# Optimization experiments

Hardware: AMD Instinct MI355X
Metric: run time of the kernel (lower is better)

The kernel has to match this reference:

```python
import jax, jax.numpy as jnp
import numpy as np

B, C, W, H, NH, FF, L = 4, 200, 300, 128, 8, 512, 2
PH = H // NH
MAXLEN = 200
PE_N = 512
NEG = -1e15


def _sinusoidal_pe():
    # fairseq-style sinusoidal table, get_embedding(512, hidden_size)
    half = H // 2
    freq = np.exp(np.arange(half, dtype=np.float64) * -(np.log(10000.0) / (half - 1)))
    ang = np.arange(PE_N, dtype=np.float64)[:, None] * freq[None, :]
    return jnp.asarray(np.concatenate([np.sin(ang), np.cos(ang)], axis=1), jnp.float32)

PE = _sinusoidal_pe()  # [512, H], frozen (requires_grad=False in torch)


def setup_inputs() -> dict:
    key = jax.random.key(0)
    ks = jax.random.split(key, 20)

    def lin(k, fan_in, shape):
        lim = 1.0 / np.sqrt(fan_in)
        return jax.random.uniform(k, shape, jnp.float32, -lim, lim)

    return {
        'chars': jax.random.normal(ks[0], (B, C, H), jnp.float32),
        'words': jax.random.normal(ks[1], (B, W, H), jnp.float32),
        'pos_s': jax.random.randint(ks[2], (B, C), 0, MAXLEN),
        'pos_e': jax.random.randint(ks[3], (B, C), 0, MAXLEN),
        'lex_s': jax.random.randint(ks[4], (B, W), 0, MAXLEN),
        'lex_e': jax.random.randint(ks[5], (B, W), 0, MAXLEN),
        'seq_len': jax.random.randint(ks[6], (B,), 100, C + 1),
        'lex_num': jax.random.randint(ks[7], (B,), 150, W + 1),
        # Four_Pos_Fusion 'ff': Linear(4H -> H) + ReLU
        'Wf': lin(ks[8], 4 * H, (4 * H, H)),
        'bf': jnp.zeros((H,), jnp.float32),
        # per-layer attention / FFN params, stacked on leading layer dim
        'Wq': lin(ks[9], H, (L, H, H)),  'bq': jnp.zeros((L, H), jnp.float32),
        'Wk': lin(ks[10], H, (L, H, H)), 'bk': jnp.zeros((L, H), jnp.float32),
        'Wv': lin(ks[11], H, (L, H, H)), 'bv': jnp.zeros((L, H), jnp.float32),
        'Wr': lin(ks[12], H, (L, H, H)), 'br': jnp.zeros((L, H), jnp.float32),
        'u_bias': jax.random.normal(ks[13], (L, NH, PH), jnp.float32) * 0.02,
        'v_bias': jax.random.normal(ks[14], (L, NH, PH), jnp.float32) * 0.02,
        'ln1_g': jnp.ones((L, H), jnp.float32), 'ln1_b': jnp.zeros((L, H), jnp.float32),
        'ln2_g': jnp.ones((L, H), jnp.float32), 'ln2_b': jnp.zeros((L, H), jnp.float32),
        'W1': lin(ks[15], H, (L, H, FF)),  'b1': jnp.zeros((L, FF), jnp.float32),
        'W2': lin(ks[16], FF, (L, FF, H)), 'b2': jnp.zeros((L, H), jnp.float32),
    }


def _ln(x, g, b):
    m = jnp.mean(x, -1, keepdims=True)
    v = jnp.var(x, -1, keepdims=True)
    return (x - m) / jnp.sqrt(v + 1e-5) * g + b


def reference(chars, words, pos_s, pos_e, lex_s, lex_e, seq_len, lex_num,
              Wf, bf, Wq, bq, Wk, bk, Wv, bv, Wr, br, u_bias, v_bias,
              ln1_g, ln1_b, ln2_g, ln2_b, W1, b1, W2, b2):
    # four relative-position distance tables (char span vs word span), offset by max_seq_len
    idx = lambda p, l: jnp.clip(p[:, :, None] - l[:, None, :] + MAXLEN, 0, PE_N - 1)
    # Linear(4H->H) over the concat of four gathered PE tensors, expressed as
    # a sum of 4 chunked matmuls to avoid materializing the [B,C,W,4H] concat.
    rel = (PE[idx(pos_s, lex_s)] @ Wf[0:H] + PE[idx(pos_s, lex_e)] @ Wf[H:2 * H]
           + PE[idx(pos_e, lex_s)] @ Wf[2 * H:3 * H] + PE[idx(pos_e, lex_e)] @ Wf[3 * H:4 * H] + bf)
    rel = jax.nn.relu(rel)  # [B, C, W, H]

    # char_lex_len_to_mask: valid (char i, word j) pairs
    mask = (jnp.arange(C) < seq_len[:, None])[:, :, None] & (jnp.arange(W) < lex_num[:, None])[:, None, :]
    mask = mask[:, None]  # [B, 1, C, W]

    out = chars
    for i in range(L):
        q = (out @ Wq[i] + bq[i]).reshape(B, C, NH, PH)
        k = (words @ Wk[i] + bk[i]).reshape(B, W, NH, PH)
        v = (words @ Wv[i] + bv[i]).reshape(B, W, NH, PH)
        r = (rel @ Wr[i] + br[i]).reshape(B, C, W, NH, PH)
        A_C = jnp.einsum('bcnp,bwnp->bncw', q + u_bias[i], k)
        B_D = jnp.einsum('bcnp,bcwnp->bncw', q + v_bias[i], r)
        score = jnp.where(mask, A_C + B_D, NEG)  # scale=False
        att = jax.nn.softmax(score, axis=-1)
        att = jnp.where(mask, att, 0.0)  # dropout=0 (eval)
        ctx = jnp.einsum('bncw,bwnp->bcnp', att, v).reshape(B, C, H)
        out = _ln(ctx + out, ln1_g[i], ln1_b[i])
        ff = jax.nn.relu(out @ W1[i] + b1[i]) @ W2[i] + b2[i]
        out = _ln(ff + out, ln2_g[i], ln2_b[i])
    return out
```

## Files before the change

kernel.cpp:

```cpp
#include <hip/hip_runtime.h>
#include <math.h>

#define B_ 4
#define C_ 200
#define CH_ 100
#define W_ 300
#define WP_ 304
#define H_ 128
#define NH_ 8
#define PH_ 16
#define FF_ 512
#define L_ 2
#define MAXLEN_ 200
#define PEN_ 512
#define WVS_ 136
#define NTILE_ 19

typedef __bf16 bf16x8 __attribute__((ext_vector_type(8)));
typedef float f32x4v __attribute__((ext_vector_type(4)));

#define SEG_PEW   64
#define SEG_KV    (SEG_PEW + 200)
#define SEG_WR    (SEG_KV + 256)
#define SEG_W1T   (SEG_WR + 128)
#define PREP_BLOCKS (SEG_W1T + 128)

__global__ __launch_bounds__(128) void prep_kernel(
        const float* __restrict__ Wf, const float* __restrict__ bfv,
        const float* __restrict__ words,
        const float* __restrict__ Wk, const float* __restrict__ bk,
        const float* __restrict__ Wv, const float* __restrict__ bv,
        const float* __restrict__ Wr, const float* __restrict__ W1,
        const float* __restrict__ W2,
        __bf16* __restrict__ kb, __bf16* __restrict__ PEWb, __bf16* __restrict__ vTb,
        __bf16* __restrict__ WrB, __bf16* __restrict__ W1T, __bf16* __restrict__ W2T) {
    __shared__ __align__(16) float s_buf[12 * H_];
    __shared__ __align__(16) __bf16 s_vt[128][12];
    __shared__ float s_tile[32][33];
    int t = threadIdx.x;
    if (blockIdx.x < SEG_PEW) {
        int p0 = blockIdx.x * 8;
        {
            int j = (t < 64) ? t : (t - 64);
            double f = exp(-(double)j * (log(10000.0) / 63.0));
            #pragma unroll
            for (int r = 0; r < 8; ++r) {
                double a = (double)(p0 + r) * f;
                s_buf[r * H_ + t] = (float)((t < 64) ? sin(a) : cos(a));
            }
        }
        __syncthreads();
        float acc0[8], acc1[8], acc2[8], acc3[8];
        #pragma unroll
        for (int r = 0; r < 8; ++r) { acc0[r] = 0.f; acc1[r] = 0.f; acc2[r] = 0.f; acc3[r] = 0.f; }
        #pragma unroll 2
        for (int j = 0; j < H_; ++j) {
            float w0 = Wf[0 * H_ * H_ + j * H_ + t];
            float w1 = Wf[1 * H_ * H_ + j * H_ + t];
            float w2 = Wf[2 * H_ * H_ + j * H_ + t];
            float w3 = Wf[3 * H_ * H_ + j * H_ + t];
            #pragma unroll
            for (int r = 0; r < 8; ++r) {
                float pv = s_buf[r * H_ + j];
                acc0[r] += pv * w0;
                acc1[r] += pv * w1;
                acc2[r] += pv * w2;
                acc3[r] += pv * w3;
            }
        }
        float bfr = bfv[t];
        #pragma unroll
        for (int r = 0; r < 8; ++r) {
            int p = p0 + r;
            PEWb[(0 * PEN_ + p) * H_ + t] = (__bf16)(acc0[r] + bfr);
            PEWb[(1 * PEN_ + p) * H_ + t] = (__bf16)acc1[r];
            PEWb[(2 * PEN_ + p) * H_ + t] = (__bf16)acc2[r];
            PEWb[(3 * PEN_ + p) * H_ + t] = (__bf16)acc3[r];
        }
    } else if (blockIdx.x < SEG_KV) {
        int idx = blockIdx.x - SEG_PEW;
        int bb = idx / 50;
        int rem = idx % 50;
        int li = rem / 25;
        int w0 = (rem % 25) * 12;
        for (int i = t; i < 12 * H_; i += 128) {
            int r = i >> 7, j = i & 127;
            s_buf[i] = words[((size_t)(bb * W_ + w0 + r)) * H_ + j];
        }
        __syncthreads();
        const float* wk = Wk + li * H_ * H_;
        const float* wv = Wv + li * H_ * H_;
        float ak[12], av[12];
        #pragma unroll
        for (int r = 0; r < 12; ++r) { ak[r] = 0.f; av[r] = 0.f; }
        #pragma unroll 2
        for (int j = 0; j < H_; ++j) {
            float kw = wk[j * H_ + t];
            float vw = wv[j * H_ + t];
            #pragma unroll
            for (int r = 0; r < 12; ++r) {
                float x = s_buf[r * H_ + j];
                ak[r] += x * kw;
                av[r] += x * vw;
            }
        }
        float bkv = bk[li * H_ + t], bvv = bv[li * H_ + t];
        #pragma unroll
        for (int r = 0; r < 12; ++r)
            kb[(size_t)(li * B_ * W_ + bb * W_ + w0 + r) * H_ + t] = (__bf16)(ak[r] + bkv);
        #pragma unroll
        for (int r = 0; r < 12; ++r) s_vt[t][r] = (__bf16)(av[r] + bvv);
        __syncthreads();
        size_t vbase = ((size_t)(li * B_ + bb) * H_) * WP_;
        for (int i = t; i < 128 * 3; i += 128) {
            int h = i / 3, ch = i % 3;
            *(uint2*)(vTb + vbase + (size_t)h * WP_ + w0 + ch * 4) =
                *(const uint2*)&s_vt[h][ch * 4];
        }
        if ((rem % 25) == 0) {
            uint2 z; z.x = 0u; z.y = 0u;
            *(uint2*)(vTb + vbase + (size_t)t * WP_ + 300) = z;
        }
    } else if (blockIdx.x < SEG_WR) {
        int i = (blockIdx.x - SEG_KV) * 128 + t;
        WrB[i] = (__bf16)Wr[i];
    } else if (blockIdx.x < SEG_W1T) {
        int blk = blockIdx.x - SEG_WR;
        int l = blk >> 6;
        int rem = blk & 63;
        int jt = rem >> 4;
        int ut = rem & 15;
        int r = t >> 5, cc = t & 31;
        #pragma unroll
        for (int k = 0; k < 8; ++k) {
            int j = jt * 32 + r + 4 * k;
            s_tile[r + 4 * k][cc] = W1[(l * H_ + j) * FF_ + ut * 32 + cc];
        }
        __syncthreads();
        int jl = t & 31, ul = t >> 5;
        #pragma unroll
        for (int k = 0; k < 8; ++k) {
            int u = ut * 32 + ul + 4 * k;
            W1T[((size_t)(l * FF_ + u)) * H_ + jt * 32 + jl] = (__bf16)s_tile[jl][ul + 4 * k];
        }
    } else {
        int blk = blockIdx.x - SEG_W1T;
        int l = blk >> 6;
        int rem = blk & 63;
        int ut = rem >> 2;
        int ht = rem & 3;
        int r = t >> 5, cc = t & 31;
        #pragma unroll
        for (int k = 0; k < 8; ++k) {
            int u = ut * 32 + r + 4 * k;
            s_tile[r + 4 * k][cc] = W2[(l * FF_ + u) * H_ + ht * 32 + cc];
        }
        __syncthreads();
        int ul = t & 31, hl = t >> 5;
        #pragma unroll
        for (int k = 0; k < 8; ++k) {
            int h = ht * 32 + hl + 4 * k;
            W2T[((size_t)(l * H_ + h)) * FF_ + ut * 32 + ul] = (__bf16)s_tile[ul][hl + 4 * k];
        }
    }
}

__global__ __launch_bounds__(256, 2) void mega_kernel(
    const float* __restrict__ chars,
    const int* __restrict__ pos_s, const int* __restrict__ pos_e,
    const int* __restrict__ lex_s, const int* __restrict__ lex_e,
    const int* __restrict__ seq_len, const int* __restrict__ lex_num,
    const float* __restrict__ Wq, const float* __restrict__ bq,
    const float* __restrict__ br,
    const float* __restrict__ u_bias, const float* __restrict__ v_bias,
    const float* __restrict__ ln1_g, const float* __restrict__ ln1_b,
    const float* __restrict__ ln2_g, const float* __restrict__ ln2_b,
    const float* __restrict__ b1, const float* __restrict__ b2,
    const __bf16* __restrict__ kb, const __bf16* __restrict__ PEWb,
    const __bf16* __restrict__ vTb, const __bf16* __restrict__ WrB,
    const __bf16* __restrict__ W1T, const __bf16* __restrict__ W2T,
    float* __restrict__ out) {

    __shared__ __align__(16) float s_x[2][H_], s_qv[2][H_];
    __shared__ __align__(16) __bf16 s_wvecb[2][16][WVS_];
    __shared__ __align__(16) __bf16 s_qub[2][16][WVS_];
    __shared__ float s_bterm[2][NH_];
    __shared__ __align__(16) float s_sc[2][NH_][WP_];
    __shared__ float s_red[2][132];
    __shared__ __align__(16) float s_hid[2][FF_];
    __shared__ float s_tmp[2][256];
    __shared__ int s_ls[W_], s_le[W_];

    int blk = blockIdx.x;
    int b = blk / CH_, c0 = blk % CH_;
    int t = threadIdx.x;
    int lane = t & 63;
    int wid = t >> 6;
    int l15 = lane & 15, quad = lane >> 4;

    if (t < H_) {
        s_x[0][t] = chars[(b * C_ + c0) * H_ + t];
        s_x[1][t] = chars[(b * C_ + c0 + CH_) * H_ + t];
    }
    for (int w = t; w < W_; w += 256) {
        s_ls[w] = lex_s[b * W_ + w];
        s_le[w] = lex_e[b * W_ + w];
    }
    for (int i = t; i < 2 * 8 * WVS_; i += 256) {
        int r = i / (8 * WVS_), rem = i % (8 * WVS_);
        s_wvecb[r][8 + rem / WVS_][rem % WVS_] = (__bf16)0.f;
    }
    for (int i = t; i < 2 * 16 * WVS_; i += 256) {
        int r = i / (16 * WVS_), rem = i % (16 * WVS_);
        s_qub[r][rem / WVS_][rem % WVS_] = (__bf16)0.f;
    }
    int ps0 = pos_s[b * C_ + c0],        pev0 = pos_e[b * C_ + c0];
    int ps1 = pos_s[b * C_ + c0 + CH_],  pev1 = pos_e[b * C_ + c0 + CH_];
    int slen = seq_len[b];
    int cvalid0 = (c0 < slen), cvalid1 = (c0 + CH_ < slen);
    int wnum = lex_num[b];
    __syncthreads();

    bf16x8 Ac0[5][4], Ac1[5][4];

    #pragma unroll
    for (int li = 0; li < L_; ++li) {
        {
            int half = t >> 7, h = t & 127;
            const float* WqL = Wq + li * H_ * H_;
            const float4* x40 = (const float4*)s_x[0];
            const float4* x41 = (const float4*)s_x[1];
            float4 a0 = {0,0,0,0}, a1 = {0,0,0,0};
            #pragma unroll 2
            for (int g = half * 16; g < half * 16 + 16; ++g) {
                float4 xa = x40[g], xb = x41[g];
                int j0 = 4 * g;
                float w0 = WqL[(j0 + 0) * H_ + h], w1 = WqL[(j0 + 1) * H_ + h];
                float w2 = WqL[(j0 + 2) * H_ + h], w3 = WqL[(j0 + 3) * H_ + h];
                a0.x += xa.x * w0; a0.y += xa.y * w1; a0.z += xa.z * w2; a0.w += xa.w * w3;
                a1.x += xb.x * w0; a1.y += xb.y * w1; a1.z += xb.z * w2; a1.w += xb.w * w3;
            }
            s_tmp[0][t] = (a0.x + a0.y) + (a0.z + a0.w);
            s_tmp[1][t] = (a1.x + a1.y) + (a1.z + a1.w);
        }
        __syncthreads();
        if (t < H_) {
            #pragma unroll
            for (int r = 0; r < 2; ++r) {
                float acc = s_tmp[r][t] + s_tmp[r][t + 128] + bq[li * H_ + t];
                s_qub[r][t >> 4][t] = (__bf16)(acc + u_bias[li * H_ + t]);
                s_qv[r][t] = acc + v_bias[li * H_ + t];
            }
        }
        __syncthreads();

        if (t < H_) {
            const __bf16* WrRow = WrB + li * H_ * H_ + t * H_;
            #pragma unroll 2
            for (int n = 0; n < NH_; ++n) {
                bf16x8 w0 = *(const bf16x8*)(WrRow + n * PH_);
                bf16x8 w1 = *(const bf16x8*)(WrRow + n * PH_ + 8);
                #pragma unroll
                for (int r = 0; r < 2; ++r) {
                    const float4* qv4 = (const float4*)(s_qv[r] + n * PH_);
                    float4 q0 = qv4[0], q1 = qv4[1], q2 = qv4[2], q3 = qv4[3];
                    float4 a4;
                    a4.x = (float)w0[0] * q0.x + (float)w1[0] * q2.x;
                    a4.y = (float)w0[1] * q0.y + (float)w1[1] * q2.y;
                    a4.z = (float)w0[2] * q0.z + (float)w1[2] * q2.z;
                    a4.w = (float)w0[3] * q0.w + (float)w1[3] * q2.w;
                    a4.x += (float)w0[4] * q1.x + (float)w1[4] * q3.x;
                    a4.y += (float)w0[5] * q1.y + (float)w1[5] * q3.y;
                    a4.z += (float)w0[6] * q1.z + (float)w1[6] * q3.z;
                    a4.w += (float)w0[7] * q1.w + (float)w1[7] * q3.w;
                    s_wvecb[r][n][t] = (__bf16)((a4.x + a4.y) + (a4.z + a4.w));
                }
            }
        } else if (t < H_ + NH_) {
            int n = t - H_;
            const float4* br4 = (const float4*)(br + li * H_ + n * PH_);
            float4 b0 = br4[0], b1v = br4[1], b2v = br4[2], b3v = br4[3];
            #pragma unroll
            for (int r = 0; r < 2; ++r) {
                const float4* qv4 = (const float4*)(s_qv[r] + n * PH_);
                float4 q0 = qv4[0], q1 = qv4[1], q2 = qv4[2], q3 = qv4[3];
                float4 a4;
                a4.x = b0.x * q0.x + b2v.x * q2.x;
                a4.y = b0.y * q0.y + b2v.y * q2.y;
                a4.z = b0.z * q0.z + b2v.z * q2.z;
                a4.w = b0.w * q0.w + b2v.w * q2.w;
                a4.x += b1v.x * q1.x + b3v.x * q3.x;
                a4.y += b1v.y * q1.y + b3v.y * q3.y;
                a4.z += b1v.z * q1.z + b3v.z * q3.z;
                a4.w += b1v.w * q1.w + b3v.w * q3.w;
                s_bterm[r][n] = (a4.x + a4.y) + (a4.z + a4.w);
            }
        }
        __syncthreads();

        const __bf16* kL = kb + (size_t)(li * B_ + b) * W_ * H_;
        {
            const __bf16* wrow0 = &s_wvecb[0][l15][0];
            const __bf16* wrow1 = &s_wvecb[1][l15][0];
            const __bf16* qrow0 = &s_qub[0][l15][0];
            const __bf16* qrow1 = &s_qub[1][l15][0];
            #pragma unroll
            for (int tc = 0; tc < 5; ++tc) {
                int tile = wid + 4 * tc;
                if (tile < NTILE_) {
                    int w0t = tile * 16;
                    int w = w0t + l15; if (w > W_ - 1) w = W_ - 1;
                    const __bf16* kr = kL + (size_t)w * H_;
                    f32x4v acc0 = {0.f,0.f,0.f,0.f}, acc1 = {0.f,0.f,0.f,0.f};
                    if (li == 0) {
                        int ls = s_ls[w], le = s_le[w];
                        int i00 = min(max(ps0 - ls + MAXLEN_, 0), PEN_ - 1);
                        int i01 = min(max(ps0 - le + MAXLEN_, 0), PEN_ - 1);
                        int i02 = min(max(pev0 - ls + MAXLEN_, 0), PEN_ - 1);
                        int i03 = min(max(pev0 - le + MAXLEN_, 0), PEN_ - 1);
                        int i10 = min(max(ps1 - ls + MAXLEN_, 0), PEN_ - 1);
                        int i11 = min(max(ps1 - le + MAXLEN_, 0), PEN_ - 1);
                        int i12 = min(max(pev1 - ls + MAXLEN_, 0), PEN_ - 1);
                        int i13 = min(max(pev1 - le + MAXLEN_, 0), PEN_ - 1);
                        const __bf16* r00 = PEWb + (size_t)(0 * PEN_ + i00) * H_;
                        const __bf16* r01 = PEWb + (size_t)(1 * PEN_ + i01) * H_;
                        const __bf16* r02 = PEWb + (size_t)(2 * PEN_ + i02) * H_;
                        const __bf16* r03 = PEWb + (size_t)(3 * PEN_ + i03) * H_;
                        const __bf16* r10 = PEWb + (size_t)(0 * PEN_ + i10) * H_;
                        const __bf16* r11 = PEWb + (size_t)(1 * PEN_ + i11) * H_;
                        const __bf16* r12 = PEWb + (size_t)(2 * PEN_ + i12) * H_;
                        const __bf16* r13 = PEWb + (size_t)(3 * PEN_ + i13) * H_;
                        #pragma unroll
                        for (int s = 0; s < 4; ++s) {
                            int h0 = s * 32 + quad * 8;
                            bf16x8 K = *(const bf16x8*)(kr + h0);
                            bf16x8 A0, A1;
                            {
                                bf16x8 t0 = *(const bf16x8*)(r00 + h0);
                                bf16x8 t1 = *(const bf16x8*)(r01 + h0);
                                bf16x8 t2 = *(const bf16x8*)(r02 + h0);
                                bf16x8 t3 = *(const bf16x8*)(r03 + h0);
                                #pragma unroll
                                for (int j = 0; j < 8; ++j)
                                    A0[j] = (__bf16)fmaxf((float)t0[j] + (float)t1[j] + (float)t2[j] + (float)t3[j], 0.f);
                            }
                            {
                                bf16x8 t0 = *(const bf16x8*)(r10 + h0);
                                bf16x8 t1 = *(const bf16x8*)(r11 + h0);
                                bf16x8 t2 = *(const bf16x8*)(r12 + h0);
                                bf16x8 t3 = *(const bf16x8*)(r13 + h0);
                                #pragma unroll
                                for (int j = 0; j < 8; ++j)
                                    A1[j] = (__bf16)fmaxf((float)t0[j] + (float)t1[j] + (float)t2[j] + (float)t3[j], 0.f);
                            }
                            Ac0[tc][s] = A0;
                            Ac1[tc][s] = A1;
                            bf16x8 Bf0 = *(const bf16x8*)(wrow0 + h0);
                            acc0 = __builtin_amdgcn_mfma_f32_16x16x32_bf16(A0, Bf0, acc0, 0, 0, 0);
                            bf16x8 Bq0 = *(const bf16x8*)(qrow0 + h0);
                            acc0 = __builtin_amdgcn_mfma_f32_16x16x32_bf16(K, Bq0, acc0, 0, 0, 0);
                            bf16x8 Bf1 = *(const bf16x8*)(wrow1 + h0);
                            acc1 = __builtin_amdgcn_mfma_f32_16x16x32_bf16(A1, Bf1, acc1, 0, 0, 0);
                            bf16x8 Bq1 = *(const bf16x8*)(qrow1 + h0);
                            acc1 = __builtin_amdgcn_mfma_f32_16x16x32_bf16(K, Bq1, acc1, 0, 0, 0);
                        }
                    } else {
                        #pragma unroll
                        for (int s = 0; s < 4; ++s) {
                            int h0 = s * 32 + quad * 8;
                            bf16x8 K = *(const bf16x8*)(kr + h0);
                            bf16x8 A0 = Ac0[tc][s];
                            bf16x8 A1 = Ac1[tc][s];
                            bf16x8 Bf0 = *(const bf16x8*)(wrow0 + h0);
                            acc0 = __builtin_amdgcn_mfma_f32_16x16x32_bf16(A0, Bf0, acc0, 0, 0, 0);
                            bf16x8 Bq0 = *(const bf16x8*)(qrow0 + h0);
                            acc0 = __builtin_amdgcn_mfma_f32_16x16x32_bf16(K, Bq0, acc0, 0, 0, 0);
                            bf16x8 Bf1 = *(const bf16x8*)(wrow1 + h0);
                            acc1 = __builtin_amdgcn_mfma_f32_16x16x32_bf16(A1, Bf1, acc1, 0, 0, 0);
                            bf16x8 Bq1 = *(const bf16x8*)(qrow1 + h0);
                            acc1 = __builtin_amdgcn_mfma_f32_16x16x32_bf16(K, Bq1, acc1, 0, 0, 0);
                        }
                    }
                    if (l15 < NH_) {
                        float bt0 = s_bterm[0][l15], bt1 = s_bterm[1][l15];
                        #pragma unroll
                        for (int r = 0; r < 4; ++r) {
                            int wr = w0t + quad * 4 + r;
                            if (wr < W_) {
                                s_sc[0][l15][wr] = acc0[r] + bt0;
                                s_sc[1][l15][wr] = acc1[r] + bt1;
                            }
                        }
                    }
                }
            }
        }
        __syncthreads();

        {
            int n = t >> 5, ln_ = t & 31;
            #pragma unroll
            for (int r = 0; r < 2; ++r) {
                int cval = r ? cvalid1 : cvalid0;
                if (cval) {
                    float m = -INFINITY;
                    for (int w = ln_; w < wnum; w += 32) m = fmaxf(m, s_sc[r][n][w]);
                    #pragma unroll
                    for (int off = 16; off > 0; off >>= 1) m = fmaxf(m, __shfl_xor(m, off, 32));
                    float sum = 0.f;
                    for (int w = ln_; w < wnum; w += 32) sum += expf(s_sc[r][n][w] - m);
                    #pragma unroll
                    for (int off = 16; off > 0; off >>= 1) sum += __shfl_xor(sum, off, 32);
                    float inv = 1.f / sum;
                    for (int w = ln_; w < WP_; w += 32)
                        s_sc[r][n][w] = (w < wnum) ? expf(s_sc[r][n][w] - m) * inv : 0.f;
                } else {
                    for (int w = ln_; w < WP_; w += 32) s_sc[r][n][w] = 0.f;
                }
            }
        }
        __syncthreads();

        {
            int h = t & 127, half = t >> 7, n = h >> 4;
            const __bf16* vrow = vTb + ((size_t)(li * B_ + b) * H_ + h) * WP_;
            const float4* att0 = (const float4*)(s_sc[0][n]);
            const float4* att1 = (const float4*)(s_sc[1][n]);
            float4 a0 = {0,0,0,0}, a1 = {0,0,0,0};
            #pragma unroll 2
            for (int g = half * 19; g < half * 19 + 19; ++g) {
                bf16x8 vv = *(const bf16x8*)(vrow + 8 * g);
                float4 p00 = att0[2 * g], p01 = att0[2 * g + 1];
                float4 p10 = att1[2 * g], p11 = att1[2 * g + 1];
                float v0 = (float)vv[0], v1 = (float)vv[1], v2 = (float)vv[2], v3 = (float)vv[3];
                float v4 = (float)vv[4], v5 = (float)vv[5], v6 = (float)vv[6], v7 = (float)vv[7];
                a0.x += p00.x * v0 + p01.x * v4;
                a0.y += p00.y * v1 + p01.y * v5;
                a0.z += p00.z * v2 + p01.z * v6;
                a0.w += p00.w * v3 + p01.w * v7;
                a1.x += p10.x * v0 + p11.x * v4;
                a1.y += p10.y * v1 + p11.y * v5;
                a1.z += p10.z * v2 + p11.z * v6;
                a1.w += p10.w * v3 + p11.w * v7;
            }
            s_tmp[0][t] = (a0.x + a0.y) + (a0.z + a0.w);
            s_tmp[1][t] = (a1.x + a1.y) + (a1.z + a1.w);
        }
        __syncthreads();

        if (t < 128) {
            s_red[0][t] = s_tmp[0][t] + s_tmp[0][t + 128] + s_x[0][t];
        } else {
            int e = t - 128;
            s_red[1][e] = s_tmp[1][e] + s_tmp[1][e + 128] + s_x[1][e];
        }
        __syncthreads();
        if (t < 128) {
            int r = t >> 6, l = t & 63;
            float a = s_red[r][l], bb = s_red[r][l + 64];
            float s = a + bb, ss = a * a + bb * bb;
            #pragma unroll
            for (int off = 32; off > 0; off >>= 1) {
                s += __shfl_down(s, off);
                ss += __shfl_down(ss, off);
            }
            if (l == 0) {
                float mean = s * (1.f / 128.f);
                float var = ss * (1.f / 128.f) - mean * mean;
                s_red[r][128] = mean;
                s_red[r][129] = rsqrtf(var + 1e-5f);
            }
        }
        __syncthreads();
        if (t < H_) {
            float g1 = ln1_g[li * H_ + t], b1v = ln1_b[li * H_ + t];
            #pragma unroll
            for (int r = 0; r < 2; ++r)
                s_x[r][t] = (s_red[r][t] - s_red[r][128]) * s_red[r][129] * g1 + b1v;
        }
        __syncthreads();

        {
            const __bf16* W1l = W1T + (size_t)li * FF_ * H_;
            int u0 = t * 2;
            const __bf16* ra = W1l + (size_t)u0 * H_;
            const __bf16* rb = W1l + (size_t)(u0 + 1) * H_;
            const float4* x40 = (const float4*)s_x[0];
            const float4* x41 = (const float4*)s_x[1];
            float4 a00 = {0,0,0,0}, a01 = {0,0,0,0}, a10 = {0,0,0,0}, a11 = {0,0,0,0};
            #pragma unroll 2
            for (int g = 0; g < 16; ++g) {
                bf16x8 wa = *(const bf16x8*)(ra + 8 * g);
                bf16x8 wb = *(const bf16x8*)(rb + 8 * g);
                float4 xa0 = x40[2 * g], xa1 = x40[2 * g + 1];
                float4 xb0 = x41[2 * g], xb1 = x41[2 * g + 1];
                a00.x += xa0.x * (float)wa[0] + xa1.x * (float)wa[4];
                a00.y += xa0.y * (float)wa[1] + xa1.y * (float)wa[5];
                a00.z += xa0.z * (float)wa[2] + xa1.z * (float)wa[6];
                a00.w += xa0.w * (float)wa[3] + xa1.w * (float)wa[7];
                a01.x += xa0.x * (float)wb[0] + xa1.x * (float)wb[4];
                a01.y += xa0.y * (float)wb[1] + xa1.y * (float)wb[5];
                a01.z += xa0.z * (float)wb[2] + xa1.z * (float)wb[6];
                a01.w += xa0.w * (float)wb[3] + xa1.w * (float)wb[7];
                a10.x += xb0.x * (float)wa[0] + xb1.x * (float)wa[4];
                a10.y += xb0.y * (float)wa[1] + xb1.y * (float)wa[5];
                a10.z += xb0.z * (float)wa[2] + xb1.z * (float)wa[6];
                a10.w += xb0.w * (float)wa[3] + xb1.w * (float)wa[7];
                a11.x += xb0.x * (float)wb[0] + xb1.x * (float)wb[4];
                a11.y += xb0.y * (float)wb[1] + xb1.y * (float)wb[5];
                a11.z += xb0.z * (float)wb[2] + xb1.z * (float)wb[6];
                a11.w += xb0.w * (float)wb[3] + xb1.w * (float)wb[7];
            }
            float bb0 = b1[li * FF_ + u0], bb1 = b1[li * FF_ + u0 + 1];
            s_hid[0][u0]     = fmaxf((a00.x + a00.y) + (a00.z + a00.w) + bb0, 0.f);
            s_hid[0][u0 + 1] = fmaxf((a01.x + a01.y) + (a01.z + a01.w) + bb1, 0.f);
            s_hid[1][u0]     = fmaxf((a10.x + a10.y) + (a10.z + a10.w) + bb0, 0.f);
            s_hid[1][u0 + 1] = fmaxf((a11.x + a11.y) + (a11.z + a11.w) + bb1, 0.f);
        }
        __syncthreads();

        {
            int half = t >> 7, h = t & 127;
            const __bf16* wrow2 = W2T + ((size_t)li * H_ + h) * FF_ + half * 256;
            const float4* h40 = (const float4*)(s_hid[0] + half * 256);
            const float4* h41 = (const float4*)(s_hid[1] + half * 256);
            float4 a0 = {0,0,0,0}, a1 = {0,0,0,0};
            #pragma unroll 2
            for (int g = 0; g < 32; ++g) {
                bf16x8 wv = *(const bf16x8*)(wrow2 + 8 * g);
                float4 p00 = h40[2 * g], p01 = h40[2 * g + 1];
                float4 p10 = h41[2 * g], p11 = h41[2 * g + 1];
                float v0 = (float)wv[0], v1 = (float)wv[1], v2 = (float)wv[2], v3 = (float)wv[3];
                float v4 = (float)wv[4], v5 = (float)wv[5], v6 = (float)wv[6], v7 = (float)wv[7];
                a0.x += p00.x * v0 + p01.x * v4;
                a0.y += p00.y * v1 + p01.y * v5;
                a0.z += p00.z * v2 + p01.z * v6;
                a0.w += p00.w * v3 + p01.w * v7;
                a1.x += p10.x * v0 + p11.x * v4;
                a1.y += p10.y * v1 + p11.y * v5;
                a1.z += p10.z * v2 + p11.z * v6;
                a1.w += p10.w * v3 + p11.w * v7;
            }
            s_tmp[0][t] = (a0.x + a0.y) + (a0.z + a0.w);
            s_tmp[1][t] = (a1.x + a1.y) + (a1.z + a1.w);
        }
        __syncthreads();

        if (t < 128) {
            s_red[0][t] = s_tmp[0][t] + s_tmp[0][t + 128] + b2[li * H_ + t] + s_x[0][t];
        } else {
            int e = t - 128;
            s_red[1][e] = s_tmp[1][e] + s_tmp[1][e + 128] + b2[li * H_ + e] + s_x[1][e];
        }
        __syncthreads();
        if (t < 128) {
            int r = t >> 6, l = t & 63;
            float a = s_red[r][l], bb = s_red[r][l + 64];
            float s = a + bb, ss = a * a + bb * bb;
            #pragma unroll
            for (int off = 32; off > 0; off >>= 1) {
                s += __shfl_down(s, off);
                ss += __shfl_down(ss, off);
            }
            if (l == 0) {
                float mean = s * (1.f / 128.f);
                float var = ss * (1.f / 128.f) - mean * mean;
                s_red[r][128] = mean;
                s_red[r][129] = rsqrtf(var + 1e-5f);
            }
        }
        __syncthreads();
        if (t < H_) {
            float g2 = ln2_g[li * H_ + t], b2v = ln2_b[li * H_ + t];
            #pragma unroll
            for (int r = 0; r < 2; ++r)
                s_x[r][t] = (s_red[r][t] - s_red[r][128]) * s_red[r][129] * g2 + b2v;
        }
        __syncthreads();
    }

    if (t < H_) {
        out[(b * C_ + c0) * H_ + t] = s_x[0][t];
        out[(b * C_ + c0 + CH_) * H_ + t] = s_x[1][t];
    }
}

extern "C" void kernel_launch(void* const* d_in, const int* in_sizes, int n_in,
                              void* d_out, int out_size, void* d_ws, size_t ws_size,
                              hipStream_t stream) {
    const float* chars  = (const float*)d_in[0];
    const float* words  = (const float*)d_in[1];
    const int* pos_s   = (const int*)d_in[2];
    const int* pos_e   = (const int*)d_in[3];
    const int* lex_s   = (const int*)d_in[4];
    const int* lex_e   = (const int*)d_in[5];
    const int* seq_len = (const int*)d_in[6];
    const int* lex_num = (const int*)d_in[7];
    const float* Wf  = (const float*)d_in[8];
    const float* bfv = (const float*)d_in[9];
    const float* Wq  = (const float*)d_in[10];
    const float* bq  = (const float*)d_in[11];
    const float* Wk  = (const float*)d_in[12];
    const float* bk  = (const float*)d_in[13];
    const float* Wv  = (const float*)d_in[14];
    const float* bv  = (const float*)d_in[15];
    const float* Wr  = (const float*)d_in[16];
    const float* br  = (const float*)d_in[17];
    const float* u_bias = (const float*)d_in[18];
    const float* v_bias = (const float*)d_in[19];
    const float* ln1_g  = (const float*)d_in[20];
    const float* ln1_b  = (const float*)d_in[21];
    const float* ln2_g  = (const float*)d_in[22];
    const float* ln2_b  = (const float*)d_in[23];
    const float* W1  = (const float*)d_in[24];
    const float* b1  = (const float*)d_in[25];
    const float* W2  = (const float*)d_in[26];
    const float* b2  = (const float*)d_in[27];

    __bf16* kb   = (__bf16*)d_ws;
    __bf16* PEWb = kb + (size_t)L_ * B_ * W_ * H_;
    __bf16* vTb  = PEWb + 4 * PEN_ * H_;
    __bf16* WrB  = vTb + (size_t)L_ * B_ * H_ * WP_;
    __bf16* W1T  = WrB + L_ * H_ * H_;
    __bf16* W2T  = W1T + L_ * H_ * FF_;

    prep_kernel<<<dim3(PREP_BLOCKS), dim3(128), 0, stream>>>(
        Wf, bfv, words, Wk, bk, Wv, bv, Wr, W1, W2,
        kb, PEWb, vTb, WrB, W1T, W2T);

    mega_kernel<<<dim3(B_ * CH_), dim3(256), 0, stream>>>(
        chars, pos_s, pos_e, lex_s, lex_e, seq_len, lex_num,
        Wq, bq, br, u_bias, v_bias,
        ln1_g, ln1_b, ln2_g, ln2_b, b1, b2,
        kb, PEWb, vTb, WrB, W1T, W2T, (float*)d_out);
}
```

Measured before the change: 245.3 us.

## Switch weight and V layouts to lane-coalesced row-major reads in mega kernel

Changes the workspace layouts so that V, W1, W2 and a transposed Wr are stored in their natural row-major orientation. The mega kernel's matvecs then read them with consecutive threads touching consecutive columns (coalesced scalar bf16 loads) instead of each thread streaming its own transposed row with 16-byte vector loads. This also simplifies the prep kernel by dropping several transposes, and the Wr projection now uses all 256 threads split across the two rows. The trade-off is more scalar load instructions and longer serial FMA chains per thread in place of vectorized per-thread row reads.

```diff
diff --git a/kernel.cpp b/kernel.cpp
--- a/kernel.cpp
+++ b/kernel.cpp
@@ -17,13 +17,14 @@
 #define NTILE_ 19
 
 typedef __bf16 bf16x8 __attribute__((ext_vector_type(8)));
+typedef __bf16 bf16x2 __attribute__((ext_vector_type(2)));
 typedef float f32x4v __attribute__((ext_vector_type(4)));
 
 #define SEG_PEW   64
 #define SEG_KV    (SEG_PEW + 200)
-#define SEG_WR    (SEG_KV + 256)
-#define SEG_W1T   (SEG_WR + 128)
-#define PREP_BLOCKS (SEG_W1T + 128)
+#define SEG_WRT   (SEG_KV + 32)
+#define SEG_CONV  (SEG_WRT + 128)
+#define PREP_BLOCKS SEG_CONV
 
 __global__ __launch_bounds__(128) void prep_kernel(
         const float* __restrict__ Wf, const float* __restrict__ bfv,
@@ -32,10 +33,9 @@
         const float* __restrict__ Wv, const float* __restrict__ bv,
         const float* __restrict__ Wr, const float* __restrict__ W1,
         const float* __restrict__ W2,
-        __bf16* __restrict__ kb, __bf16* __restrict__ PEWb, __bf16* __restrict__ vTb,
-        __bf16* __restrict__ WrB, __bf16* __restrict__ W1T, __bf16* __restrict__ W2T) {
+        __bf16* __restrict__ kb, __bf16* __restrict__ PEWb, __bf16* __restrict__ vb,
+        __bf16* __restrict__ WrT, __bf16* __restrict__ W1b, __bf16* __restrict__ W2b) {
     __shared__ __align__(16) float s_buf[12 * H_];
-    __shared__ __align__(16) __bf16 s_vt[128][12];
     __shared__ float s_tile[32][33];
     int t = threadIdx.x;
     if (blockIdx.x < SEG_PEW) {
@@ -106,61 +106,36 @@
         }
         float bkv = bk[li * H_ + t], bvv = bv[li * H_ + t];
         #pragma unroll
-        for (int r = 0; r < 12; ++r)
-            kb[(size_t)(li * B_ * W_ + bb * W_ + w0 + r) * H_ + t] = (__bf16)(ak[r] + bkv);
-        #pragma unroll
-        for (int r = 0; r < 12; ++r) s_vt[t][r] = (__bf16)(av[r] + bvv);
-        __syncthreads();
-        size_t vbase = ((size_t)(li * B_ + bb) * H_) * WP_;
-        for (int i = t; i < 128 * 3; i += 128) {
-            int h = i / 3, ch = i % 3;
-            *(uint2*)(vTb + vbase + (size_t)h * WP_ + w0 + ch * 4) =
-                *(const uint2*)&s_vt[h][ch * 4];
-        }
-        if ((rem % 25) == 0) {
-            uint2 z; z.x = 0u; z.y = 0u;
-            *(uint2*)(vTb + vbase + (size_t)t * WP_ + 300) = z;
-        }
-    } else if (blockIdx.x < SEG_WR) {
-        int i = (blockIdx.x - SEG_KV) * 128 + t;
-        WrB[i] = (__bf16)Wr[i];
-    } else if (blockIdx.x < SEG_W1T) {
-        int blk = blockIdx.x - SEG_WR;
-        int l = blk >> 6;
-        int rem = blk & 63;
-        int jt = rem >> 4;
-        int ut = rem & 15;
-        int r = t >> 5, cc = t & 31;
+        for (int r = 0; r < 12; ++r) {
+            size_t row = (size_t)(li * B_ * W_ + bb * W_ + w0 + r) * H_ + t;
+            kb[row] = (__bf16)(ak[r] + bkv);
+            vb[row] = (__bf16)(av[r] + bvv);
+        }
+    } else if (blockIdx.x < SEG_WRT) {
+        int q = blockIdx.x - SEG_KV;
+        int li = q >> 4;
+        int tile = q & 15;
+        int tr = tile >> 2, tc = tile & 3;
+        int i2 = t >> 5, j2 = t & 31;
         #pragma unroll
         for (int k = 0; k < 8; ++k) {
-            int j = jt * 32 + r + 4 * k;
-            s_tile[r + 4 * k][cc] = W1[(l * H_ + j) * FF_ + ut * 32 + cc];
-        }
-        __syncthreads();
-        int jl = t & 31, ul = t >> 5;
+            int row = tr * 32 + i2 + 4 * k;
+            s_tile[i2 + 4 * k][j2] = Wr[((size_t)(li * H_ + row)) * H_ + tc * 32 + j2];
+        }
+        __syncthreads();
         #pragma unroll
         for (int k = 0; k < 8; ++k) {
-            int u = ut * 32 + ul + 4 * k;
-            W1T[((size_t)(l * FF_ + u)) * H_ + jt * 32 + jl] = (__bf16)s_tile[jl][ul + 4 * k];
+            int o2 = i2 + 4 * k;
+            WrT[((size_t)(li * H_ + tc * 32 + o2)) * H_ + tr * 32 + j2] =
+                (__bf16)s_tile[j2][o2];
         }
     } else {
-        int blk = blockIdx.x - SEG_W1T;
-        int l = blk >> 6;
-        int rem = blk & 63;
-        int ut = rem >> 2;
-        int ht = rem & 3;
-        int r = t >> 5, cc = t & 31;
-        #pragma unroll
-        for (int k = 0; k < 8; ++k) {
-            int u = ut * 32 + r + 4 * k;
-            s_tile[r + 4 * k][cc] = W2[(l * FF_ + u) * H_ + ht * 32 + cc];
-        }
-        __syncthreads();
-        int ul = t & 31, hl = t >> 5;
-        #pragma unroll
-        for (int k = 0; k < 8; ++k) {
-            int h = ht * 32 + hl + 4 * k;
-            W2T[((size_t)(l * H_ + h)) * FF_ + ut * 32 + ul] = (__bf16)s_tile[ul][hl + 4 * k];
+        int base = (blockIdx.x - SEG_WRT) * 2048 + t;
+        #pragma unroll
+        for (int e = 0; e < 16; ++e) {
+            int idx = base + e * 128;
+            if (idx < L_ * H_ * FF_) W1b[idx] = (__bf16)W1[idx];
+            else W2b[idx - L_ * H_ * FF_] = (__bf16)W2[idx - L_ * H_ * FF_];
         }
     }
 }
@@ -177,8 +152,8 @@
     const float* __restrict__ ln2_g, const float* __restrict__ ln2_b,
     const float* __restrict__ b1, const float* __restrict__ b2,
     const __bf16* __restrict__ kb, const __bf16* __restrict__ PEWb,
-    const __bf16* __restrict__ vTb, const __bf16* __restrict__ WrB,
-    const __bf16* __restrict__ W1T, const __bf16* __restrict__ W2T,
+    const __bf16* __restrict__ vb, const __bf16* __restrict__ WrTb,
+    const __bf16* __restrict__ W1b, const __bf16* __restrict__ W2b,
     float* __restrict__ out) {
 
     __shared__ __align__(16) float s_x[2][H_], s_qv[2][H_];
@@ -254,46 +229,30 @@
         }
         __syncthreads();
 
-        if (t < H_) {
-            const __bf16* WrRow = WrB + li * H_ * H_ + t * H_;
-            #pragma unroll 2
-            for (int n = 0; n < NH_; ++n) {
-                bf16x8 w0 = *(const bf16x8*)(WrRow + n * PH_);
-                bf16x8 w1 = *(const bf16x8*)(WrRow + n * PH_ + 8);
+        {
+            int half = t >> 7, tt = t & 127;
+            const __bf16* WrTl = WrTb + (size_t)li * H_ * H_;
+            float accn[NH_];
+            #pragma unroll
+            for (int n = 0; n < NH_; ++n) accn[n] = 0.f;
+            #pragma unroll 4
+            for (int k = 0; k < PH_; ++k) {
                 #pragma unroll
-                for (int r = 0; r < 2; ++r) {
-                    const float4* qv4 = (const float4*)(s_qv[r] + n * PH_);
-                    float4 q0 = qv4[0], q1 = qv4[1], q2 = qv4[2], q3 = qv4[3];
-                    float4 a4;
-                    a4.x = (float)w0[0] * q0.x + (float)w1[0] * q2.x;
-                    a4.y = (float)w0[1] * q0.y + (float)w1[1] * q2.y;
-                    a4.z = (float)w0[2] * q0.z + (float)w1[2] * q2.z;
-                    a4.w = (float)w0[3] * q0.w + (float)w1[3] * q2.w;
-                    a4.x += (float)w0[4] * q1.x + (float)w1[4] * q3.x;
-                    a4.y += (float)w0[5] * q1.y + (float)w1[5] * q3.y;
-                    a4.z += (float)w0[6] * q1.z + (float)w1[6] * q3.z;
-                    a4.w += (float)w0[7] * q1.w + (float)w1[7] * q3.w;
-                    s_wvecb[r][n][t] = (__bf16)((a4.x + a4.y) + (a4.z + a4.w));
+                for (int n = 0; n < NH_; ++n) {
+                    float wv = (float)WrTl[(size_t)(n * PH_ + k) * H_ + tt];
+                    accn[n] += wv * s_qv[half][n * PH_ + k];
                 }
             }
-        } else if (t < H_ + NH_) {
-            int n = t - H_;
-            const float4* br4 = (const float4*)(br + li * H_ + n * PH_);
-            float4 b0 = br4[0], b1v = br4[1], b2v = br4[2], b3v = br4[3];
-            #pragma unroll
-            for (int r = 0; r < 2; ++r) {
-                const float4* qv4 = (const float4*)(s_qv[r] + n * PH_);
-                float4 q0 = qv4[0], q1 = qv4[1], q2 = qv4[2], q3 = qv4[3];
-                float4 a4;
-                a4.x = b0.x * q0.x + b2v.x * q2.x;
-                a4.y = b0.y * q0.y + b2v.y * q2.y;
-                a4.z = b0.z * q0.z + b2v.z * q2.z;
-                a4.w = b0.w * q0.w + b2v.w * q2.w;
-                a4.x += b1v.x * q1.x + b3v.x * q3.x;
-                a4.y += b1v.y * q1.y + b3v.y * q3.y;
-                a4.z += b1v.z * q1.z + b3v.z * q3.z;
-                a4.w += b1v.w * q1.w + b3v.w * q3.w;
-                s_bterm[r][n] = (a4.x + a4.y) + (a4.z + a4.w);
+            #pragma unroll
+            for (int n = 0; n < NH_; ++n)
+                s_wvecb[half][n][tt] = (__bf16)accn[n];
+            if (t < 2 * NH_) {
+                int r = t >> 3, n = t & 7;
+                float a = 0.f;
+                #pragma unroll
+                for (int k = 0; k < PH_; ++k)
+                    a += br[li * H_ + n * PH_ + k] * s_qv[r][n * PH_ + k];
+                s_bterm[r][n] = a;
             }
         }
         __syncthreads();
@@ -423,28 +382,18 @@
 
         {
             int h = t & 127, half = t >> 7, n = h >> 4;
-            const __bf16* vrow = vTb + ((size_t)(li * B_ + b) * H_ + h) * WP_;
-            const float4* att0 = (const float4*)(s_sc[0][n]);
-            const float4* att1 = (const float4*)(s_sc[1][n]);
-            float4 a0 = {0,0,0,0}, a1 = {0,0,0,0};
-            #pragma unroll 2
-            for (int g = half * 19; g < half * 19 + 19; ++g) {
-                bf16x8 vv = *(const bf16x8*)(vrow + 8 * g);
-                float4 p00 = att0[2 * g], p01 = att0[2 * g + 1];
-                float4 p10 = att1[2 * g], p11 = att1[2 * g + 1];
-                float v0 = (float)vv[0], v1 = (float)vv[1], v2 = (float)vv[2], v3 = (float)vv[3];
-                float v4 = (float)vv[4], v5 = (float)vv[5], v6 = (float)vv[6], v7 = (float)vv[7];
-                a0.x += p00.x * v0 + p01.x * v4;
-                a0.y += p00.y * v1 + p01.y * v5;
-                a0.z += p00.z * v2 + p01.z * v6;
-                a0.w += p00.w * v3 + p01.w * v7;
-                a1.x += p10.x * v0 + p11.x * v4;
-                a1.y += p10.y * v1 + p11.y * v5;
-                a1.z += p10.z * v2 + p11.z * v6;
-                a1.w += p10.w * v3 + p11.w * v7;
-            }
-            s_tmp[0][t] = (a0.x + a0.y) + (a0.z + a0.w);
-            s_tmp[1][t] = (a1.x + a1.y) + (a1.z + a1.w);
+            const __bf16* vrow = vb + ((size_t)(li * B_ + b) * W_ + half * 150) * H_ + h;
+            const float* att0 = s_sc[0][n] + half * 150;
+            const float* att1 = s_sc[1][n] + half * 150;
+            float a0 = 0.f, a1 = 0.f;
+            #pragma unroll 10
+            for (int w = 0; w < 150; ++w) {
+                float vv = (float)vrow[(size_t)w * H_];
+                a0 += att0[w] * vv;
+                a1 += att1[w] * vv;
+            }
+            s_tmp[0][t] = a0;
+            s_tmp[1][t] = a1;
         }
         __syncthreads();
 
@@ -481,68 +430,39 @@
         __syncthreads();
 
         {
-            const __bf16* W1l = W1T + (size_t)li * FF_ * H_;
+            const __bf16* W1l = W1b + (size_t)li * H_ * FF_;
             int u0 = t * 2;
-            const __bf16* ra = W1l + (size_t)u0 * H_;
-            const __bf16* rb = W1l + (size_t)(u0 + 1) * H_;
-            const float4* x40 = (const float4*)s_x[0];
-            const float4* x41 = (const float4*)s_x[1];
-            float4 a00 = {0,0,0,0}, a01 = {0,0,0,0}, a10 = {0,0,0,0}, a11 = {0,0,0,0};
-            #pragma unroll 2
-            for (int g = 0; g < 16; ++g) {
-                bf16x8 wa = *(const bf16x8*)(ra + 8 * g);
-                bf16x8 wb = *(const bf16x8*)(rb + 8 * g);
-                float4 xa0 = x40[2 * g], xa1 = x40[2 * g + 1];
-                float4 xb0 = x41[2 * g], xb1 = x41[2 * g + 1];
-                a00.x += xa0.x * (float)wa[0] + xa1.x * (float)wa[4];
-                a00.y += xa0.y * (float)wa[1] + xa1.y * (float)wa[5];
-                a00.z += xa0.z * (float)wa[2] + xa1.z * (float)wa[6];
-                a00.w += xa0.w * (float)wa[3] + xa1.w * (float)wa[7];
-                a01.x += xa0.x * (float)wb[0] + xa1.x * (float)wb[4];
-                a01.y += xa0.y * (float)wb[1] + xa1.y * (float)wb[5];
-                a01.z += xa0.z * (float)wb[2] + xa1.z * (float)wb[6];
-                a01.w += xa0.w * (float)wb[3] + xa1.w * (float)wb[7];
-                a10.x += xb0.x * (float)wa[0] + xb1.x * (float)wa[4];
-                a10.y += xb0.y * (float)wa[1] + xb1.y * (float)wa[5];
-                a10.z += xb0.z * (float)wa[2] + xb1.z * (float)wa[6];
-                a10.w += xb0.w * (float)wa[3] + xb1.w * (float)wa[7];
-                a11.x += xb0.x * (float)wb[0] + xb1.x * (float)wb[4];
-                a11.y += xb0.y * (float)wb[1] + xb1.y * (float)wb[5];
-                a11.z += xb0.z * (float)wb[2] + xb1.z * (float)wb[6];
-                a11.w += xb0.w * (float)wb[3] + xb1.w * (float)wb[7];
+            float a00 = 0.f, a01 = 0.f, a10 = 0.f, a11 = 0.f;
+            #pragma unroll 8
+            for (int j = 0; j < H_; ++j) {
+                bf16x2 wp = *(const bf16x2*)(W1l + (size_t)j * FF_ + u0);
+                float wa = (float)wp[0], wb = (float)wp[1];
+                float xa = s_x[0][j], xb = s_x[1][j];
+                a00 += xa * wa; a01 += xa * wb;
+                a10 += xb * wa; a11 += xb * wb;
             }
             float bb0 = b1[li * FF_ + u0], bb1 = b1[li * FF_ + u0 + 1];
-            s_hid[0][u0]     = fmaxf((a00.x + a00.y) + (a00.z + a00.w) + bb0, 0.f);
-            s_hid[0][u0 + 1] = fmaxf((a01.x + a01.y) + (a01.z + a01.w) + bb1, 0.f);
-            s_hid[1][u0]     = fmaxf((a10.x + a10.y) + (a10.z + a10.w) + bb0, 0.f);
-            s_hid[1][u0 + 1] = fmaxf((a11.x + a11.y) + (a11.z + a11.w) + bb1, 0.f);
-        }
-        __syncthreads();
-
-        {
-            int half = t >> 7, h = t & 127;
-            const __bf16* wrow2 = W2T + ((size_t)li * H_ + h) * FF_ + half * 256;
-            const float4* h40 = (const float4*)(s_hid[0] + half * 256);
-            const float4* h41 = (const float4*)(s_hid[1] + half * 256);
-            float4 a0 = {0,0,0,0}, a1 = {0,0,0,0};
-            #pragma unroll 2
-            for (int g = 0; g < 32; ++g) {
-                bf16x8 wv = *(const bf16x8*)(wrow2 + 8 * g);
-                float4 p00 = h40[2 * g], p01 = h40[2 * g + 1];
-                float4 p10 = h41[2 * g], p11 = h41[2 * g + 1];
-                float v0 = (float)wv[0], v1 = (float)wv[1], v2 = (float)wv[2], v3 = (float)wv[3];
-                float v4 = (float)wv[4], v5 = (float)wv[5], v6 = (float)wv[6], v7 = (float)wv[7];
-                a0.x += p00.x * v0 + p01.x * v4;
-                a0.y += p00.y * v1 + p01.y * v5;
-                a0.z += p00.z * v2 + p01.z * v6;
-                a0.w += p00.w * v3 + p01.w * v7;
-                a1.x += p10.x * v0 + p11.x * v4;
-                a1.y += p10.y * v1 + p11.y * v5;
-                a1.z += p10.z * v2 + p11.z * v6;
-                a1.w += p10.w * v3 + p11.w * v7;
-            }
-            s_tmp[0][t] = (a0.x + a0.y) + (a0.z + a0.w);
-            s_tmp[1][t] = (a1.x + a1.y) + (a1.z + a1.w);
+            s_hid[0][u0]     = fmaxf(a00 + bb0, 0.f);
+            s_hid[0][u0 + 1] = fmaxf(a01 + bb1, 0.f);
+            s_hid[1][u0]     = fmaxf(a10 + bb0, 0.f);
+            s_hid[1][u0 + 1] = fmaxf(a11 + bb1, 0.f);
+        }
+        __syncthreads();
+
+        {
+            int h = t & 127, half = t >> 7;
+            const __bf16* W2l = W2b + ((size_t)li * FF_ + half * 256) * H_ + h;
+            const float* h0 = s_hid[0] + half * 256;
+            const float* h1 = s_hid[1] + half * 256;
+            float a0 = 0.f, a1 = 0.f;
+            #pragma unroll 8
+            for (int u = 0; u < 256; ++u) {
+                float wv = (float)W2l[(size_t)u * H_];
+                a0 += h0[u] * wv;
+                a1 += h1[u] * wv;
+            }
+            s_tmp[0][t] = a0;
+            s_tmp[1][t] = a1;
         }
         __syncthreads();
 
@@ -619,18 +539,18 @@
 
     __bf16* kb   = (__bf16*)d_ws;
     __bf16* PEWb = kb + (size_t)L_ * B_ * W_ * H_;
-    __bf16* vTb  = PEWb + 4 * PEN_ * H_;
-    __bf16* WrB  = vTb + (size_t)L_ * B_ * H_ * WP_;
-    __bf16* W1T  = WrB + L_ * H_ * H_;
-    __bf16* W2T  = W1T + L_ * H_ * FF_;
+    __bf16* vb   = PEWb + 4 * PEN_ * H_;
+    __bf16* W1b  = vb + (size_t)L_ * B_ * W_ * H_;
+    __bf16* W2b  = W1b + (size_t)L_ * H_ * FF_;
+    __bf16* WrT  = W2b + (size_t)L_ * FF_ * H_;
 
     prep_kernel<<<dim3(PREP_BLOCKS), dim3(128), 0, stream>>>(
         Wf, bfv, words, Wk, bk, Wv, bv, Wr, W1, W2,
-        kb, PEWb, vTb, WrB, W1T, W2T);
+        kb, PEWb, vb, WrT, W1b, W2b);
 
     mega_kernel<<<dim3(B_ * CH_), dim3(256), 0, stream>>>(
         chars, pos_s, pos_e, lex_s, lex_e, seq_len, lex_num,
         Wq, bq, br, u_bias, v_bias,
         ln1_g, ln1_b, ln2_g, ln2_b, b1, b2,
-        kb, PEWb, vTb, WrB, W1T, W2T, (float*)d_out);
+        kb, PEWb, vb, WrT, W1b, W2b, (float*)d_out);
 }
```

Result: slower. 253.4 us (+3.3%).
